# Optimization experiments

Hardware: AMD Instinct MI355X
Metric: run time of the kernel (lower is better)

## Reference

```python
import jax, jax.numpy as jnp
import numpy as np

D = 2  # NUM_DIM (spatial dimension)


def _mlp(x, params, activate_final=False):
    n = len(params)
    for i, (w, b) in enumerate(params):
        x = x @ w + b
        if i < n - 1 or activate_final:
            x = jnp.tanh(x)
    return x


def _glorot(key, shape):
    fan_in, fan_out = shape[0], shape[-1]
    lim = np.sqrt(6.0 / (fan_in + fan_out)).astype(np.float32)
    return jax.random.uniform(key, shape, jnp.float32, -lim, lim)


def setup_inputs() -> dict:
    key = jax.random.key(0)
    ks = iter(jax.random.split(key, 40))
    B, N, M, K, P, C = 4, 32, 64, 16, 128, 2
    AW, TW, W = 64, 256, 128
    inp = {}
    inp['phase_coords'] = jax.random.normal(next(ks), (B, N, 2 * D), jnp.float32)
    inp['boundary_coords'] = jax.random.normal(next(ks), (B, M, 2 * D), jnp.float32)
    inp['boundary'] = jax.random.uniform(next(ks), (B, M), jnp.float32)
    inp['boundary_weights'] = jax.random.uniform(next(ks), (B, M), jnp.float32)
    inp['position_coords'] = jax.random.normal(next(ks), (B, P, D), jnp.float32)
    inp['sigma'] = jax.random.uniform(next(ks), (B, P, C), jnp.float32)
    inp['velocity_coords'] = jax.random.normal(next(ks), (B, K, D), jnp.float32)
    inp['velocity_weights'] = jax.random.uniform(next(ks), (B, K), jnp.float32)
    inp['scattering_kernel'] = jax.random.uniform(next(ks), (B, N, K), jnp.float32)
    inp['self_scattering_kernel'] = jax.random.uniform(next(ks), (B, K, K), jnp.float32)
    # attention MLP: input 2*D + 2 (coords ++ local frame) -> [64, 64, 1]
    inp['aw0'] = _glorot(next(ks), (2 * D + 2, AW)); inp['ab0'] = jnp.zeros((AW,), jnp.float32)
    inp['aw1'] = _glorot(next(ks), (AW, AW)); inp['ab1'] = jnp.zeros((AW,), jnp.float32)
    inp['aw2'] = _glorot(next(ks), (AW, 1)); inp['ab2'] = jnp.zeros((1,), jnp.float32)
    # transport MLP: input 4*D + C -> [256, 256, 128], activate_final=True
    inp['tw0'] = _glorot(next(ks), (4 * D + C, TW)); inp['tb0'] = jnp.zeros((TW,), jnp.float32)
    inp['tw1'] = _glorot(next(ks), (TW, TW)); inp['tb1'] = jnp.zeros((TW,), jnp.float32)
    inp['tw2'] = _glorot(next(ks), (TW, W)); inp['tb2'] = jnp.zeros((W,), jnp.float32)
    # scattering modules: res_block_depth=2 -> one stacked layer + one final layer
    inp['sw0'] = _glorot(next(ks), (W, W))
    inp['sb0'] = jax.random.uniform(next(ks), (W,), jnp.float32, -0.1, 0.1)
    inp['sw1'] = _glorot(next(ks), (W, W))
    inp['sb1'] = jax.random.uniform(next(ks), (W,), jnp.float32, -0.1, 0.1)
    inp['out_w'] = jax.random.uniform(next(ks), (W,), jnp.float32, -0.1, 0.1)
    return inp


def _forward(phase_coords, boundary_coords, boundary, boundary_weights,
             position_coords, sigma, velocity_coords, velocity_weights,
             scattering_kernel, self_scattering_kernel,
             aw0, ab0, aw1, ab1, aw2, ab2,
             tw0, tb0, tw1, tb1, tw2, tb2,
             sw0, sb0, sw1, sb1, out_w):
    B, N, _ = phase_coords.shape
    M = boundary_coords.shape[1]
    K = velocity_coords.shape[1]
    P = position_coords.shape[1]
    C = sigma.shape[-1]
    K1 = K + 1  # phase velocity v plus the Nv quadrature velocities

    x, v = phase_coords[..., :D], phase_coords[..., D:]          # (B,N,D)
    xp, vp = boundary_coords[..., :D], boundary_coords[..., D:]  # (B,M,D)

    # all velocities at which the transport MLP is evaluated: (B,N,K1,D)
    vall = jnp.concatenate(
        [v[:, :, None, :],
         jnp.broadcast_to(velocity_coords[:, None, :, :], (B, N, K, D))], axis=2)

    # ---- CoefficientNet (geometry-masked MLP attention over coeff positions) ----
    coords = jnp.concatenate(
        [jnp.broadcast_to(x[:, :, None, :], (B, N, K1, D)), vall], axis=-1)  # (B,N,K1,2D)
    ang_g = vall / jnp.sqrt(jnp.sum(vall ** 2, axis=-1, keepdims=True) + 1e-16)
    rel = x[:, :, None, :] - position_coords[:, None, :, :]                 # (B,N,P,D)
    rel_dist = jnp.sqrt(jnp.sum(rel ** 2, axis=-1) + 1e-16)                 # (B,N,P)
    pos_local = jnp.einsum('bnpd,bnkd->bnkp', rel, ang_g)                   # (B,N,K1,P)
    ang_local = pos_local / (rel_dist[:, :, None, :] + 1e-8)
    frames = jnp.stack([ang_local, pos_local], axis=-1)                     # (B,N,K1,P,2)
    qk = jnp.concatenate(
        [jnp.broadcast_to(coords[:, :, :, None, :], (B, N, K1, P, 2 * D)), frames], axis=-1)
    logits = _mlp(qk, [(aw0, ab0), (aw1, ab1), (aw2, ab2)])[..., 0]         # (B,N,K1,P)
    attn_w = jax.nn.softmax(jnp.where(pos_local > 0, logits, -1e30), axis=-1)
    coeff = jnp.exp(-jnp.einsum('bnkp,bpc->bnkc', attn_w, sigma))           # (B,N,K1,C)

    # ---- TransportModule: MLP + exp over (B,N,M,K1) ----
    t_in = jnp.concatenate([
        jnp.broadcast_to(x[:, :, None, None, :], (B, N, M, K1, D)),
        jnp.broadcast_to(vall[:, :, None, :, :], (B, N, M, K1, D)),
        jnp.broadcast_to(xp[:, None, :, None, :], (B, N, M, K1, D)),
        jnp.broadcast_to(vp[:, None, :, None, :], (B, N, M, K1, D)),
        jnp.broadcast_to(coeff[:, :, None, :, :], (B, N, M, K1, C)),
    ], axis=-1)
    g = jnp.exp(_mlp(t_in, [(tw0, tb0), (tw1, tb1), (tw2, tb2)], activate_final=True))
    act_v = g[:, :, :, 0, :]       # (B,N,M,W)  at the phase velocity
    act_vstar = g[:, :, :, 1:, :]  # (B,N,M,K,W) at the quadrature velocities

    rw_v = (1.0 - scattering_kernel) * velocity_weights[:, None, :]        # (B,N,K)
    rw_vs = (1.0 - self_scattering_kernel) * velocity_weights[:, None, :]  # (B,K,K)

    def scat_v(act, sw, sb):
        res = jnp.einsum('bnk,bnmkw->bnmw', rw_v, act)
        return jnp.tanh(jnp.einsum('iw,bnmw->bnmi', sw, res) + sb)

    def scat_vs(act, sw, sb):
        res = jnp.einsum('bij,bnmjw->bnmiw', rw_vs, act)
        return jnp.tanh(jnp.einsum('iw,bnmkw->bnmki', sw, res) + sb)

    # layer_stack block (res_block_depth - 1 = 1 layer, shared params within the layer)
    new_v = act_v + scat_v(act_vstar, sw0, sb0)
    act_vstar = act_vstar + scat_vs(act_vstar, sw0, sb0)
    act_v = new_v
    # final scattering module (fresh params) updating act_v with res_weights_v
    green = act_v + scat_v(act_vstar, sw1, sb1)

    gdot = jnp.einsum('bnmw,w->bnm', green, out_w)
    # quadrature over boundary points
    return jnp.einsum('bnm,bm->bn', gdot, boundary * boundary_weights)


def reference(phase_coords, boundary_coords, boundary, boundary_weights,
              position_coords, sigma, velocity_coords, velocity_weights,
              scattering_kernel, self_scattering_kernel,
              aw0, ab0, aw1, ab1, aw2, ab2,
              tw0, tb0, tw1, tb1, tw2, tb2,
              sw0, sb0, sw1, sb1, out_w):
    return _forward(phase_coords, boundary_coords, boundary, boundary_weights,
                    position_coords, sigma, velocity_coords, velocity_weights,
                    scattering_kernel, self_scattering_kernel,
                    aw0, ab0, aw1, ab1, aw2, ab2,
                    tw0, tb0, tw1, tb1, tw2, tb2,
                    sw0, sb0, sw1, sb1, out_w)
```

## Files before the change

### kernel.cpp

```cpp
#include <hip/hip_runtime.h>
#include <hip/hip_bf16.h>

#define BB 4
#define NN 32
#define MM 64
#define KK 16
#define KK1 17
#define PP 128
#define CC 2

typedef unsigned short ushort_t;
typedef unsigned int uint32;
typedef __attribute__((ext_vector_type(8))) short bhalf8;
typedef __attribute__((ext_vector_type(4))) float floatx4;

__device__ __forceinline__ float fast_tanh(float x) {
    float e = __expf(2.0f * x);
    return 1.0f - 2.0f / (e + 1.0f);
}
__device__ __forceinline__ ushort_t f2b(float f) {
    uint32 u = __float_as_uint(f);
    return (ushort_t)((u + 0x8000u) >> 16);
}
__device__ __forceinline__ float b2f(ushort_t h) {
    return __uint_as_float(((uint32)h) << 16);
}

__global__ void prep_kernel(const float* __restrict__ tw0, const float* __restrict__ tw1,
                            const float* __restrict__ tw2, const float* __restrict__ sw0,
                            const float* __restrict__ sw1, const float* __restrict__ aw0,
                            const float* __restrict__ aw1,
                            ushort_t* __restrict__ W0t, ushort_t* __restrict__ W1t,
                            ushort_t* __restrict__ W2t, ushort_t* __restrict__ S0t,
                            ushort_t* __restrict__ S1t, ushort_t* __restrict__ W0a,
                            ushort_t* __restrict__ W1a) {
    int i = blockIdx.x * 256 + threadIdx.x;
    if (i < 8192) {
        int nn = i >> 5, k = i & 31;
        W0t[i] = (k < 10) ? f2b(tw0[k * 256 + nn]) : (ushort_t)0;
    } else if (i < 73728) {
        int j = i - 8192; int nn = j >> 8, k = j & 255;
        W1t[j] = f2b(tw1[k * 256 + nn]);
    } else if (i < 106496) {
        int j = i - 73728; int nn = j >> 8, k = j & 255;
        W2t[j] = f2b(tw2[k * 128 + nn]);
    } else if (i < 122880) {
        S0t[i - 106496] = f2b(sw0[i - 106496]);
    } else if (i < 139264) {
        S1t[i - 122880] = f2b(sw1[i - 122880]);
    } else if (i < 141312) {
        int j = i - 139264; int nn = j >> 5, k = j & 31;
        W0a[j] = (k < 6) ? f2b(aw0[k * 64 + nn]) : (ushort_t)0;
    } else if (i < 145408) {
        int j = i - 141312; int nn = j >> 6, k = j & 63;
        W1a[j] = f2b(aw1[k * 64 + nn]);
    }
}

#define AH0S 72

__global__ __launch_bounds__(128) void attn_kernel(
    const float* __restrict__ phase, const float* __restrict__ posc,
    const float* __restrict__ sigma, const float* __restrict__ velc,
    const ushort_t* __restrict__ W0a, const ushort_t* __restrict__ W1a,
    const float* __restrict__ ab0, const float* __restrict__ ab1,
    const float* __restrict__ aw2, const float* __restrict__ ab2,
    float* __restrict__ coeff)
{
    __shared__ __align__(16) ushort_t sA0[128 * 32];
    __shared__ __align__(16) ushort_t sH0[128 * AH0S];
    __shared__ float sPL[128];
    __shared__ float sLG[128];
    __shared__ float s_red[8];

    const int tid = threadIdx.x;
    const int wave = tid >> 6;
    const int lane = tid & 63;
    const int lrow = lane & 15;
    const int lkg  = lane >> 4;

    const int blk = blockIdx.x;
    const int b = blk / (NN * KK1);
    const int rem = blk % (NN * KK1);
    const int n = rem / KK1;
    const int k = rem % KK1;

    {
        const int p = tid;
        const float x0 = phase[(b * NN + n) * 4 + 0];
        const float x1 = phase[(b * NN + n) * 4 + 1];
        float va0, va1;
        if (k == 0) { va0 = phase[(b * NN + n) * 4 + 2]; va1 = phase[(b * NN + n) * 4 + 3]; }
        else { va0 = velc[(b * KK + (k - 1)) * 2 + 0]; va1 = velc[(b * KK + (k - 1)) * 2 + 1]; }
        const float inv = rsqrtf(va0 * va0 + va1 * va1 + 1e-16f);
        const float ag0 = va0 * inv, ag1 = va1 * inv;
        const float px = posc[(b * PP + p) * 2 + 0];
        const float py = posc[(b * PP + p) * 2 + 1];
        const float r0 = x0 - px, r1 = x1 - py;
        const float rd = sqrtf(r0 * r0 + r1 * r1 + 1e-16f);
        const float pl = r0 * ag0 + r1 * ag1;
        const float al = pl / (rd + 1e-8f);
        sPL[p] = pl;
        float feat[6] = {x0, x1, va0, va1, al, pl};
        #pragma unroll
        for (int c = 0; c < 6; ++c) sA0[p * 32 + c] = f2b(feat[c]);
        #pragma unroll
        for (int c = 6; c < 32; ++c) sA0[p * 32 + c] = 0;
    }
    __syncthreads();

    {
        float b0v[4];
        #pragma unroll
        for (int j = 0; j < 4; ++j) b0v[j] = ab0[j * 16 + lrow];
        bhalf8 a[4];
        #pragma unroll
        for (int mtl = 0; mtl < 4; ++mtl)
            a[mtl] = *(const bhalf8*)&sA0[(wave * 64 + mtl * 16 + lrow) * 32 + lkg * 8];
        #pragma unroll
        for (int j = 0; j < 4; ++j) {
            bhalf8 bf = *(const bhalf8*)(W0a + (j * 16 + lrow) * 32 + lkg * 8);
            #pragma unroll
            for (int mtl = 0; mtl < 4; ++mtl) {
                floatx4 c = {0.f, 0.f, 0.f, 0.f};
                c = __builtin_amdgcn_mfma_f32_16x16x32_bf16(a[mtl], bf, c, 0, 0, 0);
                #pragma unroll
                for (int q = 0; q < 4; ++q) {
                    int row = wave * 64 + mtl * 16 + lkg * 4 + q;
                    sH0[row * AH0S + j * 16 + lrow] = f2b(fast_tanh(c[q] + b0v[j]));
                }
            }
        }
    }
    __syncthreads();

    {
        float b1v[4], w2v[4];
        #pragma unroll
        for (int j = 0; j < 4; ++j) { b1v[j] = ab1[j * 16 + lrow]; w2v[j] = aw2[j * 16 + lrow]; }
        bhalf8 a0[4], a1[4];
        #pragma unroll
        for (int mtl = 0; mtl < 4; ++mtl) {
            int base = (wave * 64 + mtl * 16 + lrow) * AH0S;
            a0[mtl] = *(const bhalf8*)&sH0[base + lkg * 8];
            a1[mtl] = *(const bhalf8*)&sH0[base + 32 + lkg * 8];
        }
        float s[4][4];
        #pragma unroll
        for (int mtl = 0; mtl < 4; ++mtl)
            #pragma unroll
            for (int q = 0; q < 4; ++q) s[mtl][q] = 0.0f;
        #pragma unroll
        for (int j = 0; j < 4; ++j) {
            bhalf8 bf0 = *(const bhalf8*)(W1a + (j * 16 + lrow) * 64 + lkg * 8);
            bhalf8 bf1 = *(const bhalf8*)(W1a + (j * 16 + lrow) * 64 + 32 + lkg * 8);
            #pragma unroll
            for (int mtl = 0; mtl < 4; ++mtl) {
                floatx4 c = {0.f, 0.f, 0.f, 0.f};
                c = __builtin_amdgcn_mfma_f32_16x16x32_bf16(a0[mtl], bf0, c, 0, 0, 0);
                c = __builtin_amdgcn_mfma_f32_16x16x32_bf16(a1[mtl], bf1, c, 0, 0, 0);
                #pragma unroll
                for (int q = 0; q < 4; ++q)
                    s[mtl][q] += fast_tanh(c[q] + b1v[j]) * w2v[j];
            }
        }
        #pragma unroll
        for (int mask = 1; mask <= 8; mask <<= 1)
            #pragma unroll
            for (int mtl = 0; mtl < 4; ++mtl)
                #pragma unroll
                for (int q = 0; q < 4; ++q)
                    s[mtl][q] += __shfl_xor(s[mtl][q], mask, 64);
        if (lrow == 0) {
            #pragma unroll
            for (int mtl = 0; mtl < 4; ++mtl)
                #pragma unroll
                for (int q = 0; q < 4; ++q)
                    sLG[wave * 64 + mtl * 16 + lkg * 4 + q] = s[mtl][q];
        }
    }
    __syncthreads();

    {
        const int p = tid;
        const float ml = (sPL[p] > 0.0f) ? (sLG[p] + ab2[0]) : -1e30f;
        const int wid = wave;
        float mv = ml;
        for (int o = 32; o > 0; o >>= 1) mv = fmaxf(mv, __shfl_xor(mv, o, 64));
        if (lane == 0) s_red[wid] = mv;
        __syncthreads();
        mv = fmaxf(s_red[0], s_red[1]);

        const float ew = __expf(ml - mv);
        float sv = ew;
        for (int o = 32; o > 0; o >>= 1) sv += __shfl_xor(sv, o, 64);
        if (lane == 0) s_red[2 + wid] = sv;
        __syncthreads();
        sv = s_red[2] + s_red[3];
        const float attn = ew / sv;

        float s0 = attn * sigma[(b * PP + p) * 2 + 0];
        float s1 = attn * sigma[(b * PP + p) * 2 + 1];
        for (int o = 32; o > 0; o >>= 1) { s0 += __shfl_xor(s0, o, 64); s1 += __shfl_xor(s1, o, 64); }
        if (lane == 0) { s_red[4 + wid] = s0; s_red[6 + wid] = s1; }
        __syncthreads();
        if (tid == 0) {
            float c0 = s_red[4] + s_red[5];
            float c1 = s_red[6] + s_red[7];
            int o = ((b * NN + n) * KK1 + k) * CC;
            coeff[o + 0] = __expf(-c0);
            coeff[o + 1] = __expf(-c1);
        }
    }
}

#define HS   264
#define GTS  56
#define AS2S 136
#define V2S  40
#define ASS  32

#define U_H0A  0
#define U_GTS  0
#define F_GV   3584
#define F_NEWV 3840
#define U_A2S  8192
#define U_H1A  8976
#define U_AS2  8976
#define U_A3   13600
#define U_A0   17952
#define U_AS   17952
#define U_V2T  18496
#define F_BBW  11808
#define F_RED  11810

__global__ __launch_bounds__(256, 3) void transport_kernel(
    const float* __restrict__ phase, const float* __restrict__ bcoord,
    const float* __restrict__ boundary, const float* __restrict__ bweights,
    const float* __restrict__ velc, const float* __restrict__ vweights,
    const float* __restrict__ scat, const float* __restrict__ selfscat,
    const float* __restrict__ coeff,
    const ushort_t* __restrict__ W0t, const ushort_t* __restrict__ W1t,
    const ushort_t* __restrict__ W2t, const ushort_t* __restrict__ S0t,
    const ushort_t* __restrict__ S1t,
    const float* __restrict__ tb0, const float* __restrict__ tb1,
    const float* __restrict__ tb2, const float* __restrict__ sb0,
    const float* __restrict__ sb1, const float* __restrict__ outw,
    float* __restrict__ out)
{
    __shared__ __align__(16) ushort_t smem[23640];
    float* smf = (float*)smem;

    const int tid = threadIdx.x;
    const int wave = tid >> 6;
    const int lane = tid & 63;
    const int lrow = lane & 15;
    const int lkg  = lane >> 4;

    const int blk = blockIdx.x;
    const int b  = blk >> 10;
    const int n  = (blk >> 5) & 31;
    const int mg = blk & 31;
    const int m0 = mg * 2;

    if (tid < 2)
        smf[F_BBW + tid] = boundary[b * MM + m0 + tid] * bweights[b * MM + m0 + tid];

    for (int idx = tid; idx < 48 * 32; idx += 256) {
        int r = idx >> 5, c = idx & 31;
        float val = 0.0f;
        if (r < 34 && c < 10) {
            int ml = (r >= 17);
            int k = r - ml * 17;
            int m = m0 + ml;
            if (c < 2)      val = phase[(b * NN + n) * 4 + c];
            else if (c < 4) val = (k == 0) ? phase[(b * NN + n) * 4 + c]
                                           : velc[(b * KK + k - 1) * 2 + (c - 2)];
            else if (c < 8) val = bcoord[(b * MM + m) * 4 + (c - 4)];
            else            val = coeff[((b * NN + n) * KK1 + k) * CC + (c - 8)];
        }
        smem[U_A0 + idx] = f2b(val);
    }
    __syncthreads();

    {
        float b0v[4];
        #pragma unroll
        for (int j = 0; j < 4; ++j) b0v[j] = tb0[(4 * wave + j) * 16 + lrow];
        bhalf8 a[3];
        #pragma unroll
        for (int mt = 0; mt < 3; ++mt)
            a[mt] = *(const bhalf8*)&smem[U_A0 + (mt * 16 + lrow) * 32 + lkg * 8];
        #pragma unroll
        for (int j = 0; j < 4; ++j) {
            int nt = 4 * wave + j;
            bhalf8 bf = *(const bhalf8*)(W0t + (nt * 16 + lrow) * 32 + lkg * 8);
            #pragma unroll
            for (int mt = 0; mt < 3; ++mt) {
                floatx4 c = {0.f, 0.f, 0.f, 0.f};
                c = __builtin_amdgcn_mfma_f32_16x16x32_bf16(a[mt], bf, c, 0, 0, 0);
                #pragma unroll
                for (int q = 0; q < 4; ++q) {
                    int row = mt * 16 + lkg * 4 + q;
                    if (row < 34)
                        smem[U_H0A + row * HS + nt * 16 + lrow] = f2b(fast_tanh(c[q] + b0v[j]));
                }
            }
        }
    }
    __syncthreads();

    for (int idx = tid; idx < 17 * 32; idx += 256) {
        int i = idx >> 5, c = idx & 31;
        float val = 0.0f;
        if (c < 16) {
            float vw = vweights[b * KK + c];
            val = (i < 16) ? (1.0f - selfscat[(b * KK + i) * KK + c]) * vw
                           : (1.0f - scat[(b * NN + n) * KK + c]) * vw;
        }
        smem[U_AS + i * ASS + c] = f2b(val);
    }
    {
        float b1v[4];
        #pragma unroll
        for (int j = 0; j < 4; ++j) b1v[j] = tb1[(4 * wave + j) * 16 + lrow];
        bhalf8 a[3][8];
        #pragma unroll
        for (int mt = 0; mt < 3; ++mt)
            #pragma unroll
            for (int ks = 0; ks < 8; ++ks)
                a[mt][ks] = *(const bhalf8*)&smem[U_H0A + (mt * 16 + lrow) * HS + ks * 32 + lkg * 8];
        #pragma unroll
        for (int j = 0; j < 4; ++j) {
            int nt = 4 * wave + j;
            const ushort_t* bp = W1t + (nt * 16 + lrow) * 256 + lkg * 8;
            floatx4 c[3];
            #pragma unroll
            for (int mt = 0; mt < 3; ++mt) c[mt] = (floatx4){0.f, 0.f, 0.f, 0.f};
            #pragma unroll
            for (int ks = 0; ks < 8; ++ks) {
                bhalf8 bf = *(const bhalf8*)(bp + ks * 32);
                #pragma unroll
                for (int mt = 0; mt < 3; ++mt)
                    c[mt] = __builtin_amdgcn_mfma_f32_16x16x32_bf16(a[mt][ks], bf, c[mt], 0, 0, 0);
            }
            #pragma unroll
            for (int mt = 0; mt < 3; ++mt)
                #pragma unroll
                for (int q = 0; q < 4; ++q) {
                    int row = mt * 16 + lkg * 4 + q;
                    if (row < 34)
                        smem[U_H1A + row * HS + nt * 16 + lrow] = f2b(fast_tanh(c[mt][q] + b1v[j]));
                }
        }
    }
    __syncthreads();

    for (int idx = tid; idx < 128 * 16; idx += 256) {
        int w = idx >> 4, r = 32 + (idx & 15);
        smem[U_GTS + w * GTS + r] = 0;
    }
    for (int idx = tid; idx < 16 * 32; idx += 256) {
        int r = idx >> 5, c = idx & 31;
        smem[U_A2S + idx] = ((c >> 4) == r) ? smem[U_AS + 16 * ASS + (c & 15)] : (ushort_t)0;
    }
    {
        float b2v[2];
        #pragma unroll
        for (int j = 0; j < 2; ++j) b2v[j] = tb2[(2 * wave + j) * 16 + lrow];
        bhalf8 a[3][8];
        #pragma unroll
        for (int mt = 0; mt < 3; ++mt)
            #pragma unroll
            for (int ks = 0; ks < 8; ++ks)
                a[mt][ks] = *(const bhalf8*)&smem[U_H1A + (mt * 16 + lrow) * HS + ks * 32 + lkg * 8];
        #pragma unroll
        for (int j = 0; j < 2; ++j) {
            int nt = 2 * wave + j;
            const ushort_t* bp = W2t + (nt * 16 + lrow) * 256 + lkg * 8;
            floatx4 c[3];
            #pragma unroll
            for (int mt = 0; mt < 3; ++mt) c[mt] = (floatx4){0.f, 0.f, 0.f, 0.f};
            #pragma unroll
            for (int ks = 0; ks < 8; ++ks) {
                bhalf8 bf = *(const bhalf8*)(bp + ks * 32);
                #pragma unroll
                for (int mt = 0; mt < 3; ++mt)
                    c[mt] = __builtin_amdgcn_mfma_f32_16x16x32_bf16(a[mt][ks], bf, c[mt], 0, 0, 0);
            }
            #pragma unroll
            for (int mt = 0; mt < 3; ++mt)
                #pragma unroll
                for (int q = 0; q < 4; ++q) {
                    int row = mt * 16 + lkg * 4 + q;
                    if (row < 34) {
                        int ml = (row >= 17);
                        int k = row - ml * 17;
                        int col = nt * 16 + lrow;
                        float g = __expf(fast_tanh(c[mt][q] + b2v[j]));
                        if (k == 0) smf[F_GV + ml * 128 + col] = g;
                        else        smem[U_GTS + col * GTS + ml * 16 + (k - 1)] = f2b(g);
                    }
                }
        }
    }
    __syncthreads();

    {
        bhalf8 a0 = *(const bhalf8*)&smem[U_AS + lrow * ASS + lkg * 8];
        bhalf8 a1 = *(const bhalf8*)&smem[U_AS + (16 + lrow) * ASS + lkg * 8];
        for (int m = 0; m < 2; ++m) {
            #pragma unroll
            for (int j = 0; j < 2; ++j) {
                int nt = 2 * wave + j;
                bhalf8 bf = *(const bhalf8*)&smem[U_GTS + (nt * 16 + lrow) * GTS + m * 16 + lkg * 8];
                #pragma unroll
                for (int mt = 0; mt < 2; ++mt) {
                    floatx4 c = {0.f, 0.f, 0.f, 0.f};
                    c = __builtin_amdgcn_mfma_f32_16x16x32_bf16(mt ? a1 : a0, bf, c, 0, 0, 0);
                    #pragma unroll
                    for (int q = 0; q < 4; ++q) {
                        int ic = mt * 16 + lkg * 4 + q;
                        if (ic < 17) {
                            int r2 = (ic == 16) ? m * 17 : m * 17 + 1 + ic;
                            smem[U_AS2 + r2 * AS2S + nt * 16 + lrow] = f2b(c[q]);
                        }
                    }
                }
            }
        }
    }
    __syncthreads();

    {
        float s0v[2];
        #pragma unroll
        for (int j = 0; j < 2; ++j) s0v[j] = sb0[(2 * wave + j) * 16 + lrow];
        bhalf8 a[3][4];
        #pragma unroll
        for (int mt = 0; mt < 3; ++mt)
            #pragma unroll
            for (int ks = 0; ks < 4; ++ks)
                a[mt][ks] = *(const bhalf8*)&smem[U_AS2 + (mt * 16 + lrow) * AS2S + ks * 32 + lkg * 8];
        #pragma unroll
        for (int j = 0; j < 2; ++j) {
            int nt = 2 * wave + j;
            const ushort_t* bp = S0t + (nt * 16 + lrow) * 128 + lkg * 8;
            floatx4 c[3];
            #pragma unroll
            for (int mt = 0; mt < 3; ++mt) c[mt] = (floatx4){0.f, 0.f, 0.f, 0.f};
            #pragma unroll
            for (int ks = 0; ks < 4; ++ks) {
                bhalf8 bf = *(const bhalf8*)(bp + ks * 32);
                #pragma unroll
                for (int mt = 0; mt < 3; ++mt)
                    c[mt] = __builtin_amdgcn_mfma_f32_16x16x32_bf16(a[mt][ks], bf, c[mt], 0, 0, 0);
            }
            #pragma unroll
            for (int mt = 0; mt < 3; ++mt)
                #pragma unroll
                for (int q = 0; q < 4; ++q) {
                    int r2 = mt * 16 + lkg * 4 + q;
                    if (r2 < 34) {
                        int m = (r2 >= 17);
                        int i2 = r2 - m * 17;
                        int col = nt * 16 + lrow;
                        float val = fast_tanh(c[mt][q] + s0v[j]);
                        if (i2 == 0) {
                            smf[F_NEWV + m * 128 + col] = smf[F_GV + m * 128 + col] + val;
                        } else {
                            int j2 = i2 - 1;
                            smem[U_V2T + col * V2S + m * 16 + j2] =
                                f2b(b2f(smem[U_GTS + col * GTS + m * 16 + j2]) + val);
                        }
                    }
                }
        }
    }
    __syncthreads();

    {
        bhalf8 a = *(const bhalf8*)&smem[U_A2S + lrow * 32 + lkg * 8];
        #pragma unroll
        for (int j = 0; j < 2; ++j) {
            int nt = 2 * wave + j;
            bhalf8 bf = *(const bhalf8*)&smem[U_V2T + (nt * 16 + lrow) * V2S + lkg * 8];
            floatx4 c = {0.f, 0.f, 0.f, 0.f};
            c = __builtin_amdgcn_mfma_f32_16x16x32_bf16(a, bf, c, 0, 0, 0);
            #pragma unroll
            for (int q = 0; q < 4; ++q) {
                int r = lkg * 4 + q;
                smem[U_A3 + r * AS2S + nt * 16 + lrow] = f2b(c[q]);
            }
        }
    }
    __syncthreads();

    float acc = 0.0f;
    {
        float s1v[2], owv[2];
        #pragma unroll
        for (int j = 0; j < 2; ++j) {
            s1v[j] = sb1[(2 * wave + j) * 16 + lrow];
            owv[j] = outw[(2 * wave + j) * 16 + lrow];
        }
        bhalf8 a[4];
        #pragma unroll
        for (int ks = 0; ks < 4; ++ks)
            a[ks] = *(const bhalf8*)&smem[U_A3 + lrow * AS2S + ks * 32 + lkg * 8];
        #pragma unroll
        for (int j = 0; j < 2; ++j) {
            int nt = 2 * wave + j;
            const ushort_t* bp = S1t + (nt * 16 + lrow) * 128 + lkg * 8;
            floatx4 c = {0.f, 0.f, 0.f, 0.f};
            #pragma unroll
            for (int ks = 0; ks < 4; ++ks) {
                bhalf8 bf = *(const bhalf8*)(bp + ks * 32);
                c = __builtin_amdgcn_mfma_f32_16x16x32_bf16(a[ks], bf, c, 0, 0, 0);
            }
            #pragma unroll
            for (int q = 0; q < 4; ++q) {
                int r = lkg * 4 + q;
                if (r < 2) {
                    int col = nt * 16 + lrow;
                    float green = smf[F_NEWV + r * 128 + col] + fast_tanh(c[q] + s1v[j]);
                    acc += green * owv[j] * smf[F_BBW + r];
                }
            }
        }
    }
    for (int o = 32; o > 0; o >>= 1) acc += __shfl_xor(acc, o, 64);
    if (lane == 0) smf[F_RED + wave] = acc;
    __syncthreads();
    if (tid == 0) {
        float tot = smf[F_RED + 0] + smf[F_RED + 1] + smf[F_RED + 2] + smf[F_RED + 3];
        atomicAdd(&out[b * NN + n], tot);
    }
}

extern "C" void kernel_launch(void* const* d_in, const int* in_sizes, int n_in,
                              void* d_out, int out_size, void* d_ws, size_t ws_size,
                              hipStream_t stream) {
    const float* phase    = (const float*)d_in[0];
    const float* bcoord   = (const float*)d_in[1];
    const float* boundary = (const float*)d_in[2];
    const float* bweights = (const float*)d_in[3];
    const float* posc     = (const float*)d_in[4];
    const float* sigma    = (const float*)d_in[5];
    const float* velc     = (const float*)d_in[6];
    const float* vweights = (const float*)d_in[7];
    const float* scat     = (const float*)d_in[8];
    const float* selfscat = (const float*)d_in[9];
    const float* aw0 = (const float*)d_in[10];
    const float* ab0 = (const float*)d_in[11];
    const float* aw1 = (const float*)d_in[12];
    const float* ab1 = (const float*)d_in[13];
    const float* aw2 = (const float*)d_in[14];
    const float* ab2 = (const float*)d_in[15];
    const float* tw0 = (const float*)d_in[16];
    const float* tb0 = (const float*)d_in[17];
    const float* tw1 = (const float*)d_in[18];
    const float* tb1 = (const float*)d_in[19];
    const float* tw2 = (const float*)d_in[20];
    const float* tb2 = (const float*)d_in[21];
    const float* sw0 = (const float*)d_in[22];
    const float* sb0 = (const float*)d_in[23];
    const float* sw1 = (const float*)d_in[24];
    const float* sb1 = (const float*)d_in[25];
    const float* outw = (const float*)d_in[26];

    float* out = (float*)d_out;
    char* ws = (char*)d_ws;
    float* coeff = (float*)ws;
    ushort_t* W0t = (ushort_t*)(ws + 17408);
    ushort_t* W1t = (ushort_t*)(ws + 33792);
    ushort_t* W2t = (ushort_t*)(ws + 164864);
    ushort_t* S0t = (ushort_t*)(ws + 230400);
    ushort_t* S1t = (ushort_t*)(ws + 263168);
    ushort_t* W0a = (ushort_t*)(ws + 295936);
    ushort_t* W1a = (ushort_t*)(ws + 300032);

    hipMemsetAsync(d_out, 0, (size_t)out_size * sizeof(float), stream);

    prep_kernel<<<568, 256, 0, stream>>>(tw0, tw1, tw2, sw0, sw1, aw0, aw1,
                                         W0t, W1t, W2t, S0t, S1t, W0a, W1a);

    attn_kernel<<<BB * NN * KK1, 128, 0, stream>>>(
        phase, posc, sigma, velc, W0a, W1a, ab0, ab1, aw2, ab2, coeff);

    transport_kernel<<<BB * NN * 32, 256, 0, stream>>>(
        phase, bcoord, boundary, bweights, velc, vweights, scat, selfscat, coeff,
        W0t, W1t, W2t, S0t, S1t, tb0, tb1, tb2, sb0, sb1, outw, out);
}
```

Before: 301.2 us.

## Factor transport first layer into per-(n,k) and per-boundary partial sums

The transport MLP's first layer is split algebraically into a term that depends on phase, velocity and coefficients (computed in the attention kernel) and a term that depends on boundary coords plus bias (computed in the prep kernel), both stored as bf16. The transport kernel then forms layer-0 activations with one add and a tanh per element, instead of running a per-block MFMA over rebuilt inputs. Layer-1 is also chunked over K to shrink LDS, F_GV/F_NEWV are stored as bf16 and launch bounds go to 4 blocks per CU. The risks are extra bf16 rounding of the partial sums and extra global traffic for the u/w workspaces.

Result: faster. 291.7 us (-3.2%).

```diff
diff --git a/kernel.cpp b/kernel.cpp
--- a/kernel.cpp
+++ b/kernel.cpp
@@ -29,31 +29,38 @@
 __global__ void prep_kernel(const float* __restrict__ tw0, const float* __restrict__ tw1,
                             const float* __restrict__ tw2, const float* __restrict__ sw0,
                             const float* __restrict__ sw1, const float* __restrict__ aw0,
-                            const float* __restrict__ aw1,
-                            ushort_t* __restrict__ W0t, ushort_t* __restrict__ W1t,
-                            ushort_t* __restrict__ W2t, ushort_t* __restrict__ S0t,
-                            ushort_t* __restrict__ S1t, ushort_t* __restrict__ W0a,
-                            ushort_t* __restrict__ W1a) {
+                            const float* __restrict__ aw1, const float* __restrict__ tb0,
+                            const float* __restrict__ bcoord,
+                            ushort_t* __restrict__ W1t, ushort_t* __restrict__ W2t,
+                            ushort_t* __restrict__ S0t, ushort_t* __restrict__ S1t,
+                            ushort_t* __restrict__ W0a, ushort_t* __restrict__ W1a,
+                            ushort_t* __restrict__ w_ws) {
     int i = blockIdx.x * 256 + threadIdx.x;
-    if (i < 8192) {
-        int nn = i >> 5, k = i & 31;
-        W0t[i] = (k < 10) ? f2b(tw0[k * 256 + nn]) : (ushort_t)0;
-    } else if (i < 73728) {
-        int j = i - 8192; int nn = j >> 8, k = j & 255;
-        W1t[j] = f2b(tw1[k * 256 + nn]);
-    } else if (i < 106496) {
-        int j = i - 73728; int nn = j >> 8, k = j & 255;
+    if (i < 65536) {
+        int nn = i >> 8, k = i & 255;
+        W1t[i] = f2b(tw1[k * 256 + nn]);
+    } else if (i < 98304) {
+        int j = i - 65536; int nn = j >> 8, k = j & 255;
         W2t[j] = f2b(tw2[k * 128 + nn]);
-    } else if (i < 122880) {
-        S0t[i - 106496] = f2b(sw0[i - 106496]);
-    } else if (i < 139264) {
-        S1t[i - 122880] = f2b(sw1[i - 122880]);
-    } else if (i < 141312) {
-        int j = i - 139264; int nn = j >> 5, k = j & 31;
+    } else if (i < 114688) {
+        S0t[i - 98304] = f2b(sw0[i - 98304]);
+    } else if (i < 131072) {
+        S1t[i - 114688] = f2b(sw1[i - 114688]);
+    } else if (i < 133120) {
+        int j = i - 131072; int nn = j >> 5, k = j & 31;
         W0a[j] = (k < 6) ? f2b(aw0[k * 64 + nn]) : (ushort_t)0;
-    } else if (i < 145408) {
-        int j = i - 141312; int nn = j >> 6, k = j & 63;
+    } else if (i < 137216) {
+        int j = i - 133120; int nn = j >> 6, k = j & 63;
         W1a[j] = f2b(aw1[k * 64 + nn]);
+    } else if (i < 202752) {
+        int j = i - 137216;
+        int m = j >> 8, c = j & 255;
+        float v = bcoord[m * 4 + 0] * tw0[4 * 256 + c]
+                + bcoord[m * 4 + 1] * tw0[5 * 256 + c]
+                + bcoord[m * 4 + 2] * tw0[6 * 256 + c]
+                + bcoord[m * 4 + 3] * tw0[7 * 256 + c]
+                + tb0[c];
+        w_ws[j] = f2b(v);
     }
 }
 
@@ -65,7 +72,7 @@
     const ushort_t* __restrict__ W0a, const ushort_t* __restrict__ W1a,
     const float* __restrict__ ab0, const float* __restrict__ ab1,
     const float* __restrict__ aw2, const float* __restrict__ ab2,
-    float* __restrict__ coeff)
+    const float* __restrict__ tw0, ushort_t* __restrict__ u_ws)
 {
     __shared__ __align__(16) ushort_t sA0[128 * 32];
     __shared__ __align__(16) ushort_t sH0[128 * AH0S];
@@ -85,11 +92,11 @@
     const int n = rem / KK1;
     const int k = rem % KK1;
 
+    float x0, x1, va0, va1;
     {
         const int p = tid;
-        const float x0 = phase[(b * NN + n) * 4 + 0];
-        const float x1 = phase[(b * NN + n) * 4 + 1];
-        float va0, va1;
+        x0 = phase[(b * NN + n) * 4 + 0];
+        x1 = phase[(b * NN + n) * 4 + 1];
         if (k == 0) { va0 = phase[(b * NN + n) * 4 + 2]; va1 = phase[(b * NN + n) * 4 + 3]; }
         else { va0 = velc[(b * KK + (k - 1)) * 2 + 0]; va1 = velc[(b * KK + (k - 1)) * 2 + 1]; }
         const float inv = rsqrtf(va0 * va0 + va1 * va1 + 1e-16f);
@@ -101,11 +108,16 @@
         const float pl = r0 * ag0 + r1 * ag1;
         const float al = pl / (rd + 1e-8f);
         sPL[p] = pl;
-        float feat[6] = {x0, x1, va0, va1, al, pl};
-        #pragma unroll
-        for (int c = 0; c < 6; ++c) sA0[p * 32 + c] = f2b(feat[c]);
-        #pragma unroll
-        for (int c = 6; c < 32; ++c) sA0[p * 32 + c] = 0;
+        bhalf8 f0;
+        f0[0] = (short)f2b(x0); f0[1] = (short)f2b(x1);
+        f0[2] = (short)f2b(va0); f0[3] = (short)f2b(va1);
+        f0[4] = (short)f2b(al); f0[5] = (short)f2b(pl);
+        f0[6] = 0; f0[7] = 0;
+        bhalf8 z = {0, 0, 0, 0, 0, 0, 0, 0};
+        *(bhalf8*)&sA0[p * 32 + 0] = f0;
+        *(bhalf8*)&sA0[p * 32 + 8] = z;
+        *(bhalf8*)&sA0[p * 32 + 16] = z;
+        *(bhalf8*)&sA0[p * 32 + 24] = z;
     }
     __syncthreads();
 
@@ -204,51 +216,51 @@
         for (int o = 32; o > 0; o >>= 1) { s0 += __shfl_xor(s0, o, 64); s1 += __shfl_xor(s1, o, 64); }
         if (lane == 0) { s_red[4 + wid] = s0; s_red[6 + wid] = s1; }
         __syncthreads();
-        if (tid == 0) {
-            float c0 = s_red[4] + s_red[5];
-            float c1 = s_red[6] + s_red[7];
-            int o = ((b * NN + n) * KK1 + k) * CC;
-            coeff[o + 0] = __expf(-c0);
-            coeff[o + 1] = __expf(-c1);
-        }
-    }
-}
-
-#define HS   264
-#define GTS  56
+
+        const float cc0 = __expf(-(s_red[4] + s_red[5]));
+        const float cc1 = __expf(-(s_red[6] + s_red[7]));
+        const int ubase = ((b * NN + n) * KK1 + k) * 256;
+        for (int cc = tid; cc < 256; cc += 128) {
+            float uv = x0 * tw0[cc] + x1 * tw0[256 + cc]
+                     + va0 * tw0[512 + cc] + va1 * tw0[768 + cc]
+                     + cc0 * tw0[2048 + cc] + cc1 * tw0[2304 + cc];
+            u_ws[ubase + cc] = f2b(uv);
+        }
+    }
+}
+
+#define H0S  136
+#define H1S  264
+#define GTSs 40
 #define AS2S 136
 #define V2S  40
-#define ASS  32
 
 #define U_H0A  0
 #define U_GTS  0
-#define F_GV   3584
-#define F_NEWV 3840
-#define U_A2S  8192
-#define U_H1A  8976
-#define U_AS2  8976
-#define U_A3   13600
-#define U_A0   17952
-#define U_AS   17952
-#define U_V2T  18496
-#define F_BBW  11808
-#define F_RED  11810
-
-__global__ __launch_bounds__(256, 3) void transport_kernel(
-    const float* __restrict__ phase, const float* __restrict__ bcoord,
+#define U_GV   5128
+#define U_NEWV 5384
+#define U_A2S  5640
+#define U_H1A  6152
+#define U_AS2  6152
+#define U_A3   6152
+#define U_AS   15128
+#define U_V2T  15128
+#define F_BBW  10128
+#define F_RED  10130
+
+__global__ __launch_bounds__(256, 4) void transport_kernel(
     const float* __restrict__ boundary, const float* __restrict__ bweights,
-    const float* __restrict__ velc, const float* __restrict__ vweights,
-    const float* __restrict__ scat, const float* __restrict__ selfscat,
-    const float* __restrict__ coeff,
-    const ushort_t* __restrict__ W0t, const ushort_t* __restrict__ W1t,
-    const ushort_t* __restrict__ W2t, const ushort_t* __restrict__ S0t,
-    const ushort_t* __restrict__ S1t,
-    const float* __restrict__ tb0, const float* __restrict__ tb1,
-    const float* __restrict__ tb2, const float* __restrict__ sb0,
-    const float* __restrict__ sb1, const float* __restrict__ outw,
+    const float* __restrict__ vweights, const float* __restrict__ scat,
+    const float* __restrict__ selfscat,
+    const ushort_t* __restrict__ W1t, const ushort_t* __restrict__ W2t,
+    const ushort_t* __restrict__ S0t, const ushort_t* __restrict__ S1t,
+    const float* __restrict__ tb1, const float* __restrict__ tb2,
+    const float* __restrict__ sb0, const float* __restrict__ sb1,
+    const float* __restrict__ outw,
+    const ushort_t* __restrict__ u_ws, const ushort_t* __restrict__ w_ws,
     float* __restrict__ out)
 {
-    __shared__ __align__(16) ushort_t smem[23640];
+    __shared__ __align__(16) ushort_t smem[20268];
     float* smf = (float*)smem;
 
     const int tid = threadIdx.x;
@@ -262,53 +274,10 @@
     const int n  = (blk >> 5) & 31;
     const int mg = blk & 31;
     const int m0 = mg * 2;
+    const int bn = b * NN + n;
 
     if (tid < 2)
         smf[F_BBW + tid] = boundary[b * MM + m0 + tid] * bweights[b * MM + m0 + tid];
-
-    for (int idx = tid; idx < 48 * 32; idx += 256) {
-        int r = idx >> 5, c = idx & 31;
-        float val = 0.0f;
-        if (r < 34 && c < 10) {
-            int ml = (r >= 17);
-            int k = r - ml * 17;
-            int m = m0 + ml;
-            if (c < 2)      val = phase[(b * NN + n) * 4 + c];
-            else if (c < 4) val = (k == 0) ? phase[(b * NN + n) * 4 + c]
-                                           : velc[(b * KK + k - 1) * 2 + (c - 2)];
-            else if (c < 8) val = bcoord[(b * MM + m) * 4 + (c - 4)];
-            else            val = coeff[((b * NN + n) * KK1 + k) * CC + (c - 8)];
-        }
-        smem[U_A0 + idx] = f2b(val);
-    }
-    __syncthreads();
-
-    {
-        float b0v[4];
-        #pragma unroll
-        for (int j = 0; j < 4; ++j) b0v[j] = tb0[(4 * wave + j) * 16 + lrow];
-        bhalf8 a[3];
-        #pragma unroll
-        for (int mt = 0; mt < 3; ++mt)
-            a[mt] = *(const bhalf8*)&smem[U_A0 + (mt * 16 + lrow) * 32 + lkg * 8];
-        #pragma unroll
-        for (int j = 0; j < 4; ++j) {
-            int nt = 4 * wave + j;
-            bhalf8 bf = *(const bhalf8*)(W0t + (nt * 16 + lrow) * 32 + lkg * 8);
-            #pragma unroll
-            for (int mt = 0; mt < 3; ++mt) {
-                floatx4 c = {0.f, 0.f, 0.f, 0.f};
-                c = __builtin_amdgcn_mfma_f32_16x16x32_bf16(a[mt], bf, c, 0, 0, 0);
-                #pragma unroll
-                for (int q = 0; q < 4; ++q) {
-                    int row = mt * 16 + lkg * 4 + q;
-                    if (row < 34)
-                        smem[U_H0A + row * HS + nt * 16 + lrow] = f2b(fast_tanh(c[q] + b0v[j]));
-                }
-            }
-        }
-    }
-    __syncthreads();
 
     for (int idx = tid; idx < 17 * 32; idx += 256) {
         int i = idx >> 5, c = idx & 31;
@@ -316,78 +285,92 @@
         if (c < 16) {
             float vw = vweights[b * KK + c];
             val = (i < 16) ? (1.0f - selfscat[(b * KK + i) * KK + c]) * vw
-                           : (1.0f - scat[(b * NN + n) * KK + c]) * vw;
-        }
-        smem[U_AS + i * ASS + c] = f2b(val);
-    }
-    {
-        float b1v[4];
-        #pragma unroll
-        for (int j = 0; j < 4; ++j) b1v[j] = tb1[(4 * wave + j) * 16 + lrow];
-        bhalf8 a[3][8];
-        #pragma unroll
-        for (int mt = 0; mt < 3; ++mt)
-            #pragma unroll
-            for (int ks = 0; ks < 8; ++ks)
-                a[mt][ks] = *(const bhalf8*)&smem[U_H0A + (mt * 16 + lrow) * HS + ks * 32 + lkg * 8];
+                           : (1.0f - scat[bn * KK + c]) * vw;
+        }
+        smem[U_AS + idx] = f2b(val);
+    }
+
+    floatx4 c1[4][3];
+    #pragma unroll
+    for (int j = 0; j < 4; ++j)
+        #pragma unroll
+        for (int mt = 0; mt < 3; ++mt) c1[j][mt] = (floatx4){0.f, 0.f, 0.f, 0.f};
+
+    for (int chunk = 0; chunk < 2; ++chunk) {
+        if (chunk) __syncthreads();
+        for (int idx = tid; idx < 34 * 16; idx += 256) {
+            int row = idx >> 4, oct = idx & 15;
+            int ml = (row >= 17);
+            int k = row - ml * 17;
+            bhalf8 uu = *(const bhalf8*)(u_ws + (bn * KK1 + k) * 256 + chunk * 128 + oct * 8);
+            bhalf8 ww = *(const bhalf8*)(w_ws + (b * MM + m0 + ml) * 256 + chunk * 128 + oct * 8);
+            bhalf8 hh;
+            #pragma unroll
+            for (int jj = 0; jj < 8; ++jj)
+                hh[jj] = (short)f2b(fast_tanh(b2f((ushort_t)uu[jj]) + b2f((ushort_t)ww[jj])));
+            *(bhalf8*)&smem[U_H0A + row * H0S + oct * 8] = hh;
+        }
+        __syncthreads();
+        #pragma unroll
+        for (int ksl = 0; ksl < 4; ++ksl) {
+            bhalf8 a[3];
+            #pragma unroll
+            for (int mt = 0; mt < 3; ++mt)
+                a[mt] = *(const bhalf8*)&smem[U_H0A + (mt * 16 + lrow) * H0S + ksl * 32 + lkg * 8];
+            #pragma unroll
+            for (int j = 0; j < 4; ++j) {
+                bhalf8 bf = *(const bhalf8*)(W1t + ((4 * wave + j) * 16 + lrow) * 256
+                                             + chunk * 128 + ksl * 32 + lkg * 8);
+                #pragma unroll
+                for (int mt = 0; mt < 3; ++mt)
+                    c1[j][mt] = __builtin_amdgcn_mfma_f32_16x16x32_bf16(a[mt], bf, c1[j][mt], 0, 0, 0);
+            }
+        }
+    }
+    {
         #pragma unroll
         for (int j = 0; j < 4; ++j) {
-            int nt = 4 * wave + j;
-            const ushort_t* bp = W1t + (nt * 16 + lrow) * 256 + lkg * 8;
-            floatx4 c[3];
-            #pragma unroll
-            for (int mt = 0; mt < 3; ++mt) c[mt] = (floatx4){0.f, 0.f, 0.f, 0.f};
-            #pragma unroll
-            for (int ks = 0; ks < 8; ++ks) {
-                bhalf8 bf = *(const bhalf8*)(bp + ks * 32);
-                #pragma unroll
-                for (int mt = 0; mt < 3; ++mt)
-                    c[mt] = __builtin_amdgcn_mfma_f32_16x16x32_bf16(a[mt][ks], bf, c[mt], 0, 0, 0);
-            }
+            float bb = tb1[(4 * wave + j) * 16 + lrow];
             #pragma unroll
             for (int mt = 0; mt < 3; ++mt)
                 #pragma unroll
                 for (int q = 0; q < 4; ++q) {
                     int row = mt * 16 + lkg * 4 + q;
                     if (row < 34)
-                        smem[U_H1A + row * HS + nt * 16 + lrow] = f2b(fast_tanh(c[mt][q] + b1v[j]));
+                        smem[U_H1A + row * H1S + (4 * wave + j) * 16 + lrow] =
+                            f2b(fast_tanh(c1[j][mt][q] + bb));
                 }
         }
     }
     __syncthreads();
 
-    for (int idx = tid; idx < 128 * 16; idx += 256) {
-        int w = idx >> 4, r = 32 + (idx & 15);
-        smem[U_GTS + w * GTS + r] = 0;
-    }
-    for (int idx = tid; idx < 16 * 32; idx += 256) {
-        int r = idx >> 5, c = idx & 31;
-        smem[U_A2S + idx] = ((c >> 4) == r) ? smem[U_AS + 16 * ASS + (c & 15)] : (ushort_t)0;
-    }
-    {
-        float b2v[2];
-        #pragma unroll
-        for (int j = 0; j < 2; ++j) b2v[j] = tb2[(2 * wave + j) * 16 + lrow];
-        bhalf8 a[3][8];
-        #pragma unroll
-        for (int mt = 0; mt < 3; ++mt)
-            #pragma unroll
-            for (int ks = 0; ks < 8; ++ks)
-                a[mt][ks] = *(const bhalf8*)&smem[U_H1A + (mt * 16 + lrow) * HS + ks * 32 + lkg * 8];
+    for (int idx = tid; idx < 1032; idx += 256) {
+        int pos = (idx < 1024) ? ((idx >> 3) * GTSs + 32 + (idx & 7)) : (5120 + idx - 1024);
+        smem[U_GTS + pos] = 0;
+    }
+    {
+        floatx4 c2[2][3];
+        #pragma unroll
+        for (int j = 0; j < 2; ++j)
+            #pragma unroll
+            for (int mt = 0; mt < 3; ++mt) c2[j][mt] = (floatx4){0.f, 0.f, 0.f, 0.f};
+        #pragma unroll
+        for (int ks = 0; ks < 8; ++ks) {
+            bhalf8 a[3];
+            #pragma unroll
+            for (int mt = 0; mt < 3; ++mt)
+                a[mt] = *(const bhalf8*)&smem[U_H1A + (mt * 16 + lrow) * H1S + ks * 32 + lkg * 8];
+            #pragma unroll
+            for (int j = 0; j < 2; ++j) {
+                bhalf8 bf = *(const bhalf8*)(W2t + ((2 * wave + j) * 16 + lrow) * 256 + ks * 32 + lkg * 8);
+                #pragma unroll
+                for (int mt = 0; mt < 3; ++mt)
+                    c2[j][mt] = __builtin_amdgcn_mfma_f32_16x16x32_bf16(a[mt], bf, c2[j][mt], 0, 0, 0);
+            }
+        }
         #pragma unroll
         for (int j = 0; j < 2; ++j) {
-            int nt = 2 * wave + j;
-            const ushort_t* bp = W2t + (nt * 16 + lrow) * 256 + lkg * 8;
-            floatx4 c[3];
-            #pragma unroll
-            for (int mt = 0; mt < 3; ++mt) c[mt] = (floatx4){0.f, 0.f, 0.f, 0.f};
-            #pragma unroll
-            for (int ks = 0; ks < 8; ++ks) {
-                bhalf8 bf = *(const bhalf8*)(bp + ks * 32);
-                #pragma unroll
-                for (int mt = 0; mt < 3; ++mt)
-                    c[mt] = __builtin_amdgcn_mfma_f32_16x16x32_bf16(a[mt][ks], bf, c[mt], 0, 0, 0);
-            }
+            float bb = tb2[(2 * wave + j) * 16 + lrow];
             #pragma unroll
             for (int mt = 0; mt < 3; ++mt)
                 #pragma unroll
@@ -396,24 +379,28 @@
                     if (row < 34) {
                         int ml = (row >= 17);
                         int k = row - ml * 17;
-                        int col = nt * 16 + lrow;
-                        float g = __expf(fast_tanh(c[mt][q] + b2v[j]));
-                        if (k == 0) smf[F_GV + ml * 128 + col] = g;
-                        else        smem[U_GTS + col * GTS + ml * 16 + (k - 1)] = f2b(g);
+                        int col = (2 * wave + j) * 16 + lrow;
+                        float g = __expf(fast_tanh(c2[j][mt][q] + bb));
+                        if (k == 0) smem[U_GV + ml * 128 + col] = f2b(g);
+                        else        smem[U_GTS + col * GTSs + ml * 16 + (k - 1)] = f2b(g);
                     }
                 }
         }
     }
     __syncthreads();
 
-    {
-        bhalf8 a0 = *(const bhalf8*)&smem[U_AS + lrow * ASS + lkg * 8];
-        bhalf8 a1 = *(const bhalf8*)&smem[U_AS + (16 + lrow) * ASS + lkg * 8];
+    for (int idx = tid; idx < 512; idx += 256) {
+        int r = idx >> 5, c = idx & 31;
+        smem[U_A2S + idx] = ((c >> 4) == r) ? smem[U_AS + 16 * 32 + (c & 15)] : (ushort_t)0;
+    }
+    {
+        bhalf8 a0 = *(const bhalf8*)&smem[U_AS + lrow * 32 + lkg * 8];
+        bhalf8 a1 = *(const bhalf8*)&smem[U_AS + (16 + lrow) * 32 + lkg * 8];
         for (int m = 0; m < 2; ++m) {
             #pragma unroll
             for (int j = 0; j < 2; ++j) {
                 int nt = 2 * wave + j;
-                bhalf8 bf = *(const bhalf8*)&smem[U_GTS + (nt * 16 + lrow) * GTS + m * 16 + lkg * 8];
+                bhalf8 bf = *(const bhalf8*)&smem[U_GTS + (nt * 16 + lrow) * GTSs + m * 16 + lkg * 8];
                 #pragma unroll
                 for (int mt = 0; mt < 2; ++mt) {
                     floatx4 c = {0.f, 0.f, 0.f, 0.f};
@@ -433,29 +420,28 @@
     __syncthreads();
 
     {
-        float s0v[2];
-        #pragma unroll
-        for (int j = 0; j < 2; ++j) s0v[j] = sb0[(2 * wave + j) * 16 + lrow];
-        bhalf8 a[3][4];
-        #pragma unroll
-        for (int mt = 0; mt < 3; ++mt)
-            #pragma unroll
-            for (int ks = 0; ks < 4; ++ks)
-                a[mt][ks] = *(const bhalf8*)&smem[U_AS2 + (mt * 16 + lrow) * AS2S + ks * 32 + lkg * 8];
+        floatx4 c3[2][3];
+        #pragma unroll
+        for (int j = 0; j < 2; ++j)
+            #pragma unroll
+            for (int mt = 0; mt < 3; ++mt) c3[j][mt] = (floatx4){0.f, 0.f, 0.f, 0.f};
+        #pragma unroll
+        for (int ks = 0; ks < 4; ++ks) {
+            bhalf8 a[3];
+            #pragma unroll
+            for (int mt = 0; mt < 3; ++mt)
+                a[mt] = *(const bhalf8*)&smem[U_AS2 + (mt * 16 + lrow) * AS2S + ks * 32 + lkg * 8];
+            #pragma unroll
+            for (int j = 0; j < 2; ++j) {
+                bhalf8 bf = *(const bhalf8*)(S0t + ((2 * wave + j) * 16 + lrow) * 128 + ks * 32 + lkg * 8);
+                #pragma unroll
+                for (int mt = 0; mt < 3; ++mt)
+                    c3[j][mt] = __builtin_amdgcn_mfma_f32_16x16x32_bf16(a[mt], bf, c3[j][mt], 0, 0, 0);
+            }
+        }
         #pragma unroll
         for (int j = 0; j < 2; ++j) {
-            int nt = 2 * wave + j;
-            const ushort_t* bp = S0t + (nt * 16 + lrow) * 128 + lkg * 8;
-            floatx4 c[3];
-            #pragma unroll
-            for (int mt = 0; mt < 3; ++mt) c[mt] = (floatx4){0.f, 0.f, 0.f, 0.f};
-            #pragma unroll
-            for (int ks = 0; ks < 4; ++ks) {
-                bhalf8 bf = *(const bhalf8*)(bp + ks * 32);
-                #pragma unroll
-                for (int mt = 0; mt < 3; ++mt)
-                    c[mt] = __builtin_amdgcn_mfma_f32_16x16x32_bf16(a[mt][ks], bf, c[mt], 0, 0, 0);
-            }
+            float bb = sb0[(2 * wave + j) * 16 + lrow];
             #pragma unroll
             for (int mt = 0; mt < 3; ++mt)
                 #pragma unroll
@@ -464,14 +450,15 @@
                     if (r2 < 34) {
                         int m = (r2 >= 17);
                         int i2 = r2 - m * 17;
-                        int col = nt * 16 + lrow;
-                        float val = fast_tanh(c[mt][q] + s0v[j]);
+                        int col = (2 * wave + j) * 16 + lrow;
+                        float val = fast_tanh(c3[j][mt][q] + bb);
                         if (i2 == 0) {
-                            smf[F_NEWV + m * 128 + col] = smf[F_GV + m * 128 + col] + val;
+                            smem[U_NEWV + m * 128 + col] =
+                                f2b(b2f(smem[U_GV + m * 128 + col]) + val);
                         } else {
                             int j2 = i2 - 1;
                             smem[U_V2T + col * V2S + m * 16 + j2] =
-                                f2b(b2f(smem[U_GTS + col * GTS + m * 16 + j2]) + val);
+                                f2b(b2f(smem[U_GTS + col * GTSs + m * 16 + j2]) + val);
                         }
                     }
                 }
@@ -498,12 +485,6 @@
 
     float acc = 0.0f;
     {
-        float s1v[2], owv[2];
-        #pragma unroll
-        for (int j = 0; j < 2; ++j) {
-            s1v[j] = sb1[(2 * wave + j) * 16 + lrow];
-            owv[j] = outw[(2 * wave + j) * 16 + lrow];
-        }
         bhalf8 a[4];
         #pragma unroll
         for (int ks = 0; ks < 4; ++ks)
@@ -511,11 +492,12 @@
         #pragma unroll
         for (int j = 0; j < 2; ++j) {
             int nt = 2 * wave + j;
-            const ushort_t* bp = S1t + (nt * 16 + lrow) * 128 + lkg * 8;
+            float s1v = sb1[nt * 16 + lrow];
+            float owv = outw[nt * 16 + lrow];
             floatx4 c = {0.f, 0.f, 0.f, 0.f};
             #pragma unroll
             for (int ks = 0; ks < 4; ++ks) {
-                bhalf8 bf = *(const bhalf8*)(bp + ks * 32);
+                bhalf8 bf = *(const bhalf8*)(S1t + (nt * 16 + lrow) * 128 + ks * 32 + lkg * 8);
                 c = __builtin_amdgcn_mfma_f32_16x16x32_bf16(a[ks], bf, c, 0, 0, 0);
             }
             #pragma unroll
@@ -523,8 +505,8 @@
                 int r = lkg * 4 + q;
                 if (r < 2) {
                     int col = nt * 16 + lrow;
-                    float green = smf[F_NEWV + r * 128 + col] + fast_tanh(c[q] + s1v[j]);
-                    acc += green * owv[j] * smf[F_BBW + r];
+                    float green = b2f(smem[U_NEWV + r * 128 + col]) + fast_tanh(c[q] + s1v);
+                    acc += green * owv * smf[F_BBW + r];
                 }
             }
         }
@@ -534,7 +516,7 @@
     __syncthreads();
     if (tid == 0) {
         float tot = smf[F_RED + 0] + smf[F_RED + 1] + smf[F_RED + 2] + smf[F_RED + 3];
-        atomicAdd(&out[b * NN + n], tot);
+        atomicAdd(&out[bn], tot);
     }
 }
 
@@ -571,24 +553,24 @@
 
     float* out = (float*)d_out;
     char* ws = (char*)d_ws;
-    float* coeff = (float*)ws;
-    ushort_t* W0t = (ushort_t*)(ws + 17408);
-    ushort_t* W1t = (ushort_t*)(ws + 33792);
-    ushort_t* W2t = (ushort_t*)(ws + 164864);
-    ushort_t* S0t = (ushort_t*)(ws + 230400);
-    ushort_t* S1t = (ushort_t*)(ws + 263168);
-    ushort_t* W0a = (ushort_t*)(ws + 295936);
-    ushort_t* W1a = (ushort_t*)(ws + 300032);
+    ushort_t* W1t  = (ushort_t*)(ws + 0);
+    ushort_t* W2t  = (ushort_t*)(ws + 131072);
+    ushort_t* S0t  = (ushort_t*)(ws + 196608);
+    ushort_t* S1t  = (ushort_t*)(ws + 229376);
+    ushort_t* W0a  = (ushort_t*)(ws + 262144);
+    ushort_t* W1a  = (ushort_t*)(ws + 266240);
+    ushort_t* u_ws = (ushort_t*)(ws + 274432);
+    ushort_t* w_ws = (ushort_t*)(ws + 1388544);
 
     hipMemsetAsync(d_out, 0, (size_t)out_size * sizeof(float), stream);
 
-    prep_kernel<<<568, 256, 0, stream>>>(tw0, tw1, tw2, sw0, sw1, aw0, aw1,
-                                         W0t, W1t, W2t, S0t, S1t, W0a, W1a);
+    prep_kernel<<<792, 256, 0, stream>>>(tw0, tw1, tw2, sw0, sw1, aw0, aw1, tb0, bcoord,
+                                         W1t, W2t, S0t, S1t, W0a, W1a, w_ws);
 
     attn_kernel<<<BB * NN * KK1, 128, 0, stream>>>(
-        phase, posc, sigma, velc, W0a, W1a, ab0, ab1, aw2, ab2, coeff);
+        phase, posc, sigma, velc, W0a, W1a, ab0, ab1, aw2, ab2, tw0, u_ws);
 
     transport_kernel<<<BB * NN * 32, 256, 0, stream>>>(
-        phase, bcoord, boundary, bweights, velc, vweights, scat, selfscat, coeff,
-        W0t, W1t, W2t, S0t, S1t, tb0, tb1, tb2, sb0, sb1, outw, out);
-}
+        boundary, bweights, vweights, scat, selfscat,
+        W1t, W2t, S0t, S1t, tb1, tb2, sb0, sb1, outw, u_ws, w_ws, out);
+}
```
